# Kernel tuning notes

Measured on AMD Instinct MI355X. Metric: run time of the kernel, lower is better.

The kernel has to match this reference:

```python
import jax, jax.numpy as jnp
import numpy as np

_CLIP_MIN = 1e-6
_POS_ALPHA = 1e-3
RADIUS = 3
HALF_D = RADIUS * RADIUS  # 9: patch vector length per class
N_FINE, N_MID, N_HIGH = 19, 7, 3
LAMBDA = 0.5
LOSS_WEIGHT = 1.0
IGNORE = 255

_F2M = np.array([0,0,0,1,1,1,2,2,3,3,4,5,5,6,6,6,6,6,6], dtype=np.int64)
_M2H = np.array([0,0,1,1,1,2,2], dtype=np.int64)
_F2H = _M2H[_F2M]


def setup_inputs():
    key = jax.random.key(0)
    k1, k2, k3, k4 = jax.random.split(key, 4)
    B, H, W, D = 4, 512, 512, 256
    return {
        "step": 5000,
        "embedding": jax.random.normal(k1, (B, D, H // 8, W // 8), jnp.float32),
        "cls_score_before": jax.random.normal(k2, (B, N_FINE, H // 8, W // 8), jnp.float32),
        "cls_score": jax.random.normal(k3, (B, N_FINE + N_MID + N_HIGH, H, W), jnp.float32),
        "label": jax.random.randint(k4, (B, H, W), 0, N_FINE),
        "fine_to_mid": jnp.asarray(_F2M),
        "fine_to_high": jnp.asarray(_F2H),
    }


def _maxpool3(x):  # kernel=stride=3, VALID (rmi_pool_way=0)
    return jax.lax.reduce_window(x, -jnp.inf, jax.lax.max, (1, 1, 3, 3), (1, 1, 3, 3), "VALID")


def _map_get_pairs(la, pr, radius=RADIUS):
    b, c, h, w = la.shape
    nh, nw = h - radius + 1, w - radius + 1
    las = [la[:, :, y:y + nh, x:x + nw] for y in range(radius) for x in range(radius)]
    prs = [pr[:, :, y:y + nh, x:x + nw] for y in range(radius) for x in range(radius)]
    la_v = jnp.stack(las, axis=2).reshape(b, c, radius * radius, nh * nw)
    pr_v = jnp.stack(prs, axis=2).reshape(b, c, radius * radius, nh * nw)
    return la_v, pr_v


def _rmi_lower_bound(oh, probs, vmask):
    # oh, probs: [B,C,H,W]; vmask: [B,1,H,W]
    la = _maxpool3(oh * vmask)
    pr = _maxpool3(probs * vmask + _CLIP_MIN)
    la_v, pr_v = _map_get_pairs(la, pr)  # [B,C,half_d,N]
    la_v = jax.lax.stop_gradient(la_v)   # labels are detached in the original
    la_v = la_v - la_v.mean(axis=-1, keepdims=True)
    pr_v = pr_v - pr_v.mean(axis=-1, keepdims=True)
    diag = _POS_ALPHA * jnp.eye(HALF_D, dtype=la_v.dtype)
    pr_cov = jnp.einsum("bcdn,bcen->bcde", pr_v, pr_v) + diag
    la_cov = jnp.einsum("bcdn,bcen->bcde", la_v, la_v)
    la_pr = jnp.einsum("bcdn,bcen->bcde", la_v, pr_v)
    appro = la_cov - la_pr @ jnp.linalg.solve(pr_cov, jnp.swapaxes(la_pr, -1, -2)) + diag
    chol = jnp.linalg.cholesky(appro)
    logdet = 2.0 * jnp.sum(jnp.log(jnp.diagonal(chol, axis1=-2, axis2=-1) + 1e-8), axis=-1)  # [B,C]
    return jnp.sum(logdet.mean(axis=0) / HALF_D)


def _hiera_bce(oh, pos, neg, vmask):
    # positives judged against min-combined probs, negatives against max-combined probs
    loss = -(oh * jnp.log(pos + 1e-8) + (1.0 - oh) * jnp.log(1.0 - neg + 1e-8)) * vmask
    return loss.sum() / (vmask.sum() * oh.shape[1] + 1e-8)


def _forward(cls_score, label, fine_to_mid, fine_to_high):
    probs = jax.nn.sigmoid(cls_score.astype(jnp.float32))
    valid = (label != IGNORE)
    vmask = valid[:, None].astype(jnp.float32)  # [B,1,H,W]
    lf = jnp.where(valid, label, 0)
    lm = fine_to_mid[lf]
    lh = fine_to_high[lf]
    oh_f = jax.nn.one_hot(lf, N_FINE, axis=1, dtype=jnp.float32)
    oh_m = jax.nn.one_hot(lm, N_MID, axis=1, dtype=jnp.float32)
    oh_h = jax.nn.one_hot(lh, N_HIGH, axis=1, dtype=jnp.float32)
    MCMA = probs[:, :N_FINE]
    MCMB = probs[:, N_FINE:N_FINE + N_MID]
    MCMC = probs[:, N_FINE + N_MID:]
    # upward (max) hierarchy consistency
    segf = jax.ops.segment_max(jnp.moveaxis(MCMA, 1, 0), fine_to_mid, num_segments=N_MID)
    MCMB_c = jnp.maximum(jnp.moveaxis(segf, 0, 1), MCMB)
    mid_to_high = jnp.zeros((N_MID,), dtype=fine_to_high.dtype).at[fine_to_mid].set(fine_to_high)
    segm = jax.ops.segment_max(jnp.moveaxis(MCMB_c, 1, 0), mid_to_high, num_segments=N_HIGH)
    MCMC_c = jnp.maximum(jnp.moveaxis(segm, 0, 1), MCMC)
    # downward (min) hierarchy consistency
    MCLA = jnp.minimum(MCMA, MCMB[:, fine_to_mid])
    MCLB_c = jnp.minimum(MCMB, MCMC[:, mid_to_high])
    MCLC_c = MCMC
    total = 0.0
    for oh, pos, neg in ((oh_f, MCLA, MCMA), (oh_m, MCLB_c, MCMB_c), (oh_h, MCLC_c, MCMC_c)):
        bce = _hiera_bce(oh, pos, neg, vmask)
        rmi = _rmi_lower_bound(oh, pos, vmask)
        total = total + LAMBDA * bce + (1.0 - LAMBDA) * rmi
    return LOSS_WEIGHT * total


def reference(step, embedding, cls_score_before, cls_score, label, fine_to_mid, fine_to_high):
    # step / embedding / cls_score_before feed only the triplet branch (not in provided source)
    return _forward(cls_score, label, fine_to_mid, fine_to_high)
```

## Files before the change

### kernel.cpp

```cpp
#include <hip/hip_runtime.h>
#include <math.h>

namespace {
constexpr int NB = 4, NCHT = 29, NF = 19, NM = 7, NHI = 3;
constexpr int HH = 512, WW = 512;
constexpr int PH  = 170;
constexpr int NHW = 168;
constexpr int NS  = NHW * NHW;
constexpr int NBC = NB * NCHT;
constexpr int CROWS = 14;
constexpr int NCH2  = NHW / CROWS;

constexpr int F2M[NF] = {0,0,0,1,1,1,2,2,3,3,4,5,5,6,6,6,6,6,6};
constexpr int M2H[NM] = {0,0,1,1,1,2,2};
constexpr int F2H[NF] = {0,0,0,0,0,0,1,1,1,1,1,2,2,2,2,2,2,2,2};

constexpr unsigned long long packTbl(const int* a, int n) {
  unsigned long long p = 0;
  for (int i = 0; i < n; i++) p |= (unsigned long long)(a[i]) << (3 * i);
  return p;
}
constexpr unsigned long long PF2M = packTbl(F2M, NF);
constexpr unsigned long long PF2H = packTbl(F2H, NF);

constexpr int    WS_S1  = 16;
constexpr int    WS_COV = 4096;
constexpr int    WS_RED = 49152;
constexpr size_t WS_LA  = 65536;
constexpr size_t WS_PR  = WS_LA + (size_t)NBC * PH * PH;
constexpr size_t WS_ZERO_BYTES = (size_t)(WS_RED + 64 * 16) * 4;
}

#define GLOAD16(gsrc, ldst)                                                     \
  __builtin_amdgcn_global_load_lds(                                             \
      (const __attribute__((address_space(1))) void*)(gsrc),                    \
      (__attribute__((address_space(3))) void*)(ldst), 16, 0, 0)

__global__ __launch_bounds__(192)
void kA(const float* __restrict__ cls, const int* __restrict__ label,
        float* __restrict__ ws) {
  const int bx  = blockIdx.x;
  const int wy  = blockIdx.y;
  const int b   = blockIdx.z;
  const int tid = threadIdx.x;
  const int x0  = 48 * bx;
  const int y0  = 3 * wy;
  const int rmax = (wy == 170) ? 1 : 2;

  const int W4   = (bx < 10) ? 12 : 8;
  const int NCOL = 4 * W4;
  const int CST  = 3 * NCOL;
  const int NW   = (bx < 10) ? 16 : 10;

  __shared__ __align__(16) float    sPixF[NCHT * 144];
  __shared__ unsigned sMask[144];
  __shared__ float    sRed[4][3];

  {
    const int T3 = 3 * W4;
    const int total = NCHT * T3;
    for (int i = tid; i < total; i += 192) {
      const int c   = i / T3;
      const int rem = i - c * T3;
      const int r   = rem / W4;
      const int f   = rem - r * W4;
      const int rr  = (r <= rmax) ? r : rmax;
      const float* src =
          cls + ((size_t)(b * NCHT + c) * HH + (y0 + rr)) * WW + x0 + 4 * f;
      GLOAD16(src, &sPixF[4 * i]);
    }
  }
  __syncthreads();

  float bce0 = 0.f, bce1 = 0.f, bce2 = 0.f, cnt = 0.f;
  {
    const int p = tid;
    const int r = p / NCOL;
    if (p < CST && r <= rmax) {
      const int col = p - r * NCOL;
      const int lbl = label[((size_t)b * HH + (y0 + r)) * WW + x0 + col];
      const bool valid = (lbl != 255);
      const int lf = valid ? lbl : 0;
      const int lm = (int)((PF2M >> (3 * lf)) & 7ull);
      const int lh = (int)((PF2H >> (3 * lf)) & 7ull);
      const float vm = valid ? 1.f : 0.f;

      float pv[NCHT];
      #pragma unroll
      for (int c = 0; c < NCHT; c++)
        pv[c] = __builtin_amdgcn_rcpf(1.f + __expf(-sPixF[c * CST + p]));

      float segf[NM];
      #pragma unroll
      for (int m = 0; m < NM; m++) segf[m] = -1.f;
      #pragma unroll
      for (int f = 0; f < NF; f++) segf[F2M[f]] = fmaxf(segf[F2M[f]], pv[f]);
      float pBc[NM];
      #pragma unroll
      for (int m = 0; m < NM; m++) pBc[m] = fmaxf(segf[m], pv[NF + m]);
      float segm[NHI];
      #pragma unroll
      for (int k = 0; k < NHI; k++) segm[k] = -1.f;
      #pragma unroll
      for (int m = 0; m < NM; m++) segm[M2H[m]] = fmaxf(segm[M2H[m]], pBc[m]);
      float pCc[NHI];
      #pragma unroll
      for (int k = 0; k < NHI; k++) pCc[k] = fmaxf(segm[k], pv[NF + NM + k]);

      #pragma unroll
      for (int f = 0; f < NF; f++) {
        const float pos = fminf(pv[f], pv[NF + F2M[f]]);
        if (valid)
          bce0 -= __logf((f == lf) ? pos + 1e-8f : 1.f - pv[f] + 1e-8f);
        sPixF[f * CST + p] = pos * vm + 1e-6f;
      }
      #pragma unroll
      for (int m = 0; m < NM; m++) {
        const float pos = fminf(pv[NF + m], pv[NF + NM + M2H[m]]);
        if (valid)
          bce1 -= __logf((m == lm) ? pos + 1e-8f : 1.f - pBc[m] + 1e-8f);
        sPixF[(NF + m) * CST + p] = pos * vm + 1e-6f;
      }
      #pragma unroll
      for (int k = 0; k < NHI; k++) {
        const float pos = pv[NF + NM + k];
        if (valid)
          bce2 -= __logf((k == lh) ? pos + 1e-8f : 1.f - pCc[k] + 1e-8f);
        sPixF[(NF + NM + k) * CST + p] = pos * vm + 1e-6f;
      }
      sMask[p] = valid ? ((1u << lf) | (1u << (19 + lm)) | (1u << (26 + lh))) : 0u;
      cnt = vm;
    }
  }

  #pragma unroll
  for (int m = 32; m >= 1; m >>= 1) {
    bce0 += __shfl_xor(bce0, m);
    bce1 += __shfl_xor(bce1, m);
    bce2 += __shfl_xor(bce2, m);
    cnt  += __shfl_xor(cnt, m);
  }
  {
    const int wave = tid >> 6, lane = tid & 63;
    if (lane == 0) {
      sRed[0][wave] = bce0; sRed[1][wave] = bce1;
      sRed[2][wave] = bce2; sRed[3][wave] = cnt;
    }
  }
  __syncthreads();

  if (wy < 170) {
    float* la = ws + WS_LA;
    float* pr = ws + WS_PR;
    for (int t = tid; t < 16 * NCHT; t += 192) {
      const int c = t >> 4;
      const int w = t & 15;
      if (w < NW) {
        const int c0 = 3 * w;
        unsigned m = 0u;
        #pragma unroll
        for (int r = 0; r < 3; r++)
          m |= sMask[r * NCOL + c0] | sMask[r * NCOL + c0 + 1] |
               sMask[r * NCOL + c0 + 2];
        const size_t base =
            ((size_t)(b * NCHT) * PH + wy) * PH + (16 * bx + w);
        la[base + (size_t)c * PH * PH] = (float)((m >> c) & 1u);
        float v = 0.f;
        #pragma unroll
        for (int r = 0; r < 3; r++)
          v = fmaxf(v, fmaxf(fmaxf(sPixF[c * CST + r * NCOL + c0],
                                   sPixF[c * CST + r * NCOL + c0 + 1]),
                             sPixF[c * CST + r * NCOL + c0 + 2]));
        pr[base + (size_t)c * PH * PH] = v;
      }
    }
  }

  if (tid == 0) {
    const int slot = (bx + 11 * (wy + 171 * b)) & 63;
    float* dst = ws + WS_RED + slot * 16;
    atomicAdd(&dst[0], sRed[0][0] + sRed[0][1] + sRed[0][2]);
    atomicAdd(&dst[1], sRed[1][0] + sRed[1][1] + sRed[1][2]);
    atomicAdd(&dst[2], sRed[2][0] + sRed[2][1] + sRed[2][2]);
    atomicAdd(&dst[3], sRed[3][0] + sRed[3][1] + sRed[3][2]);
  }
}

__global__ __launch_bounds__(192)
void kCov(const float* __restrict__ ws_base, float* __restrict__ cov,
          float* __restrict__ s1out) {
  const int bc    = blockIdx.x / NCH2;
  const int chunk = blockIdx.x % NCH2;
  const int tid   = threadIdx.x;
  const int tile  = tid / 32;
  const int g     = tid % 32;
  const int ta = (tile < 3) ? 0 : ((tile < 5) ? 1 : 2);
  const int tb = (tile < 3) ? tile : ((tile < 5) ? tile - 2 : 2);
  const bool diag = (ta == tb);

  __shared__ __align__(16) float sA[16 * PH];
  __shared__ __align__(16) float sP[16 * PH];

  const int r0 = chunk * CROWS;
  const float* Ag = ws_base + WS_LA + (size_t)bc * PH * PH + (size_t)r0 * PH;
  const float* Pg = ws_base + WS_PR + (size_t)bc * PH * PH + (size_t)r0 * PH;
  for (int i = tid; i < (16 * PH) / 4; i += 192) {
    GLOAD16(Ag + 4 * i, &sA[4 * i]);
    GLOAD16(Pg + 4 * i, &sP[4 * i]);
  }
  __syncthreads();

  const float* baseA[6];
  const float* baseB[6];
  #pragma unroll
  for (int k = 0; k < 6; k++) {
    int r = 6 * ta + k, rr = r % 9;
    baseA[k] = ((r < 9) ? sA : sP) + (rr / 3) * PH + (rr % 3);
    int r2 = 6 * tb + k, rr2 = r2 % 9;
    baseB[k] = ((r2 < 9) ? sA : sP) + (rr2 / 3) * PH + (rr2 % 3);
  }

  float acc[6][6];
  #pragma unroll
  for (int k = 0; k < 6; k++)
    #pragma unroll
    for (int l = 0; l < 6; l++) acc[k][l] = 0.f;
  float sums[6];
  #pragma unroll
  for (int k = 0; k < 6; k++) sums[k] = 0.f;

  for (int lr = 0; lr < CROWS; lr++) {
    const int rowoff = lr * PH;
    for (int lc = g; lc < NHW; lc += 32) {
      float va[6], vb[6];
      #pragma unroll
      for (int k = 0; k < 6; k++) va[k] = baseA[k][rowoff + lc];
      #pragma unroll
      for (int k = 0; k < 6; k++) vb[k] = baseB[k][rowoff + lc];
      #pragma unroll
      for (int k = 0; k < 6; k++)
        #pragma unroll
        for (int l = 0; l < 6; l++) acc[k][l] = fmaf(va[k], vb[l], acc[k][l]);
      if (diag) {
        #pragma unroll
        for (int k = 0; k < 6; k++) sums[k] += va[k];
      }
    }
  }

  #pragma unroll
  for (int k = 0; k < 6; k++)
    #pragma unroll
    for (int l = 0; l < 6; l++) {
      float v = acc[k][l];
      #pragma unroll
      for (int m = 16; m >= 1; m >>= 1) v += __shfl_xor(v, m);
      acc[k][l] = v;
    }
  if (diag) {
    #pragma unroll
    for (int k = 0; k < 6; k++) {
      float v = sums[k];
      #pragma unroll
      for (int m = 16; m >= 1; m >>= 1) v += __shfl_xor(v, m);
      sums[k] = v;
    }
  }
  if (g == 0) {
    float* dst = cov + (size_t)bc * 324;
    #pragma unroll
    for (int k = 0; k < 6; k++)
      #pragma unroll
      for (int l = 0; l < 6; l++)
        atomicAdd(&dst[(6 * ta + k) * 18 + 6 * tb + l], acc[k][l]);
    if (diag) {
      #pragma unroll
      for (int k = 0; k < 6; k++)
        atomicAdd(&s1out[bc * 32 + 6 * ta + k], sums[k]);
    }
  }
}

__global__ __launch_bounds__(64)
void kSolve(const float* __restrict__ cov_all, const float* __restrict__ s1,
            float* __restrict__ acc) {
  const int bc   = blockIdx.x;
  const int lane = threadIdx.x;
  const float* cr = cov_all + (size_t)bc * 324;
  const double n = (double)NS;

  double mu[18];
  #pragma unroll
  for (int r = 0; r < 18; r++) mu[r] = (double)s1[bc * 32 + r] / n;
#define CC(i, j) ((double)cr[(i) * 18 + (j)] - n * mu[(i)] * mu[(j)])

  double row[9];
  #pragma unroll
  for (int j = 0; j < 9; j++)
    row[j] = (lane < 9 && j <= lane) ? CC(9 + j, 9 + lane) : 0.0;
  if (lane < 9) row[lane] += 1e-3;

  #pragma unroll
  for (int k = 0; k < 9; k++) {
    if (lane == k) {
      double s = row[k];
      #pragma unroll
      for (int m = 0; m < k; m++) s -= row[m] * row[m];
      row[k] = sqrt(fmax(s, 1e-300));
    }
    double rk[9];
    #pragma unroll
    for (int m = 0; m <= k; m++) rk[m] = __shfl(row[m], k);
    if (lane > k && lane < 9) {
      double s = row[k];
      #pragma unroll
      for (int m = 0; m < k; m++) s -= row[m] * rk[m];
      row[k] = s / rk[k];
    }
  }

  double Lm[9][9];
  #pragma unroll
  for (int i = 0; i < 9; i++)
    #pragma unroll
    for (int m = 0; m <= i; m++) Lm[i][m] = __shfl(row[m], i);

  double mc[9];
  #pragma unroll
  for (int r = 0; r < 9; r++) mc[r] = 0.0;
  if (lane < 9) {
    #pragma unroll
    for (int r = 0; r < 9; r++) {
      double s = CC(lane, 9 + r);
      #pragma unroll
      for (int m = 0; m < r; m++) s -= Lm[r][m] * mc[m];
      mc[r] = s / Lm[r][r];
    }
  }

  double a2[9];
  #pragma unroll
  for (int j = 0; j < 9; j++) a2[j] = 0.0;
  #pragma unroll
  for (int j = 0; j < 9; j++) {
    double mj[9];
    #pragma unroll
    for (int r = 0; r < 9; r++) mj[r] = __shfl(mc[r], j);
    double dot = 0.0;
    #pragma unroll
    for (int r = 0; r < 9; r++) dot += mc[r] * mj[r];
    if (lane < 9 && j <= lane)
      a2[j] = CC(j, lane) - dot + ((j == lane) ? 1e-3 : 0.0);
  }
#undef CC

  double myld = 0.0;
  #pragma unroll
  for (int k = 0; k < 9; k++) {
    if (lane == k) {
      double s = a2[k];
      #pragma unroll
      for (int m = 0; m < k; m++) s -= a2[m] * a2[m];
      double d = sqrt(fmax(s, 0.0));
      a2[k] = d;
      myld = 2.0 * log(d + 1e-8);
    }
    double rk[9];
    #pragma unroll
    for (int m = 0; m <= k; m++) rk[m] = __shfl(a2[m], k);
    if (lane > k && lane < 9) {
      double s = a2[k];
      #pragma unroll
      for (int m = 0; m < k; m++) s -= a2[m] * rk[m];
      a2[k] = s / rk[k];
    }
  }
  #pragma unroll
  for (int m = 32; m >= 1; m >>= 1) myld += __shfl_xor(myld, m);
  if (lane == 0) atomicAdd(&acc[4], (float)myld);
}

__global__ void kFin(const float* __restrict__ ws, float* __restrict__ out) {
  const int tid = threadIdx.x;
  const float* slot = ws + WS_RED + tid * 16;
  float b0 = slot[0], b1 = slot[1], b2 = slot[2], b3 = slot[3];
  #pragma unroll
  for (int m = 32; m >= 1; m >>= 1) {
    b0 += __shfl_xor(b0, m);
    b1 += __shfl_xor(b1, m);
    b2 += __shfl_xor(b2, m);
    b3 += __shfl_xor(b3, m);
  }
  if (tid == 0) {
    const double cnt = (double)b3;
    const double bce = 0.5 * ((double)b0 / (cnt * NF + 1e-8) +
                              (double)b1 / (cnt * NM + 1e-8) +
                              (double)b2 / (cnt * NHI + 1e-8));
    const double rmi = 0.5 * (double)ws[4] / (double)(NB * 9);
    out[0] = (float)(bce + rmi);
  }
}

extern "C" void kernel_launch(void* const* d_in, const int* in_sizes, int n_in,
                              void* d_out, int out_size, void* d_ws, size_t ws_size,
                              hipStream_t stream) {
  (void)in_sizes; (void)n_in; (void)out_size; (void)ws_size;
  const float* cls   = (const float*)d_in[3];
  const int*   label = (const int*)d_in[4];
  float* ws = (float*)d_ws;

  hipMemsetAsync(d_ws, 0, WS_ZERO_BYTES, stream);

  dim3 gA(11, 171, NB);
  kA<<<gA, 192, 0, stream>>>(cls, label, ws);
  kCov<<<NBC * NCH2, 192, 0, stream>>>(ws, ws + WS_COV, ws + WS_S1);
  kSolve<<<NBC, 64, 0, stream>>>(ws + WS_COV, ws + WS_S1, ws);
  kFin<<<1, 64, 0, stream>>>(ws, (float*)d_out);
}
```

Baseline: 126.8 us.

## Pool logits before sigmoid, use product-of-exp BCE, and tile pooled plane layout

The first kernel now max-pools raw logits and applies the sigmoid only to each pooled value, relying on sigmoid being monotonic. This cuts the per-pixel sigmoids to one per pooled cell. BCE is rewritten as log(1+exp(±x)) terms accumulated as products, so each group needs one log instead of one log per class. The pooled label and prediction planes move to a tiled layout (block × batch-channel × 16) so the writes are contiguous per block, and the covariance kernel gathers rows from that layout into padded LDS rows. Kernel A is also templated on tile width so the constants are known at compile time. Risks include float overflow of the accumulated products when logits are large, and scattered 16-byte gathers in the covariance load.

```diff
diff --git a/kernel.cpp b/kernel.cpp
--- a/kernel.cpp
+++ b/kernel.cpp
@@ -10,24 +10,26 @@
 constexpr int NBC = NB * NCHT;
 constexpr int CROWS = 14;
 constexpr int NCH2  = NHW / CROWS;
+constexpr int LDSW  = 176;
 
 constexpr int F2M[NF] = {0,0,0,1,1,1,2,2,3,3,4,5,5,6,6,6,6,6,6};
 constexpr int M2H[NM] = {0,0,1,1,1,2,2};
-constexpr int F2H[NF] = {0,0,0,0,0,0,1,1,1,1,1,2,2,2,2,2,2,2,2};
 
 constexpr unsigned long long packTbl(const int* a, int n) {
   unsigned long long p = 0;
   for (int i = 0; i < n; i++) p |= (unsigned long long)(a[i]) << (3 * i);
   return p;
 }
+constexpr int F2H_[NF] = {0,0,0,0,0,0,1,1,1,1,1,2,2,2,2,2,2,2,2};
 constexpr unsigned long long PF2M = packTbl(F2M, NF);
-constexpr unsigned long long PF2H = packTbl(F2H, NF);
+constexpr unsigned long long PF2H = packTbl(F2H_, NF);
 
 constexpr int    WS_S1  = 16;
 constexpr int    WS_COV = 4096;
 constexpr int    WS_RED = 49152;
+constexpr size_t PLANEF = (size_t)170 * 11 * NBC * 16;
 constexpr size_t WS_LA  = 65536;
-constexpr size_t WS_PR  = WS_LA + (size_t)NBC * PH * PH;
+constexpr size_t WS_PR  = WS_LA + PLANEF;
 constexpr size_t WS_ZERO_BYTES = (size_t)(WS_RED + 64 * 16) * 4;
 }
 
@@ -36,48 +38,35 @@
       (const __attribute__((address_space(1))) void*)(gsrc),                    \
       (__attribute__((address_space(3))) void*)(ldst), 16, 0, 0)
 
-__global__ __launch_bounds__(192)
-void kA(const float* __restrict__ cls, const int* __restrict__ label,
-        float* __restrict__ ws) {
-  const int bx  = blockIdx.x;
-  const int wy  = blockIdx.y;
-  const int b   = blockIdx.z;
-  const int tid = threadIdx.x;
-  const int x0  = 48 * bx;
-  const int y0  = 3 * wy;
+template <int W4>
+__device__ __forceinline__ void kA_body(
+    const int bx, const int wy, const int b, const int tid,
+    const float* __restrict__ cls, const int* __restrict__ label,
+    float* __restrict__ ws, float* sPixF, unsigned* sMask, float (*sRed)[3]) {
+  constexpr int NCOL = 4 * W4;
+  constexpr int CST  = 3 * NCOL;
+  constexpr int T3   = 3 * W4;
+  const int x0   = 48 * bx;
+  const int y0   = 3 * wy;
   const int rmax = (wy == 170) ? 1 : 2;
 
-  const int W4   = (bx < 10) ? 12 : 8;
-  const int NCOL = 4 * W4;
-  const int CST  = 3 * NCOL;
-  const int NW   = (bx < 10) ? 16 : 10;
-
-  __shared__ __align__(16) float    sPixF[NCHT * 144];
-  __shared__ unsigned sMask[144];
-  __shared__ float    sRed[4][3];
-
-  {
-    const int T3 = 3 * W4;
-    const int total = NCHT * T3;
-    for (int i = tid; i < total; i += 192) {
-      const int c   = i / T3;
-      const int rem = i - c * T3;
-      const int r   = rem / W4;
-      const int f   = rem - r * W4;
-      const int rr  = (r <= rmax) ? r : rmax;
-      const float* src =
-          cls + ((size_t)(b * NCHT + c) * HH + (y0 + rr)) * WW + x0 + 4 * f;
-      GLOAD16(src, &sPixF[4 * i]);
-    }
+  for (int i = tid; i < NCHT * T3; i += 192) {
+    const int c   = i / T3;
+    const int rem = i - c * T3;
+    const int r   = rem / W4;
+    const int f   = rem - r * W4;
+    const int rr  = (r <= rmax) ? r : rmax;
+    const float* src =
+        cls + ((size_t)(b * NCHT + c) * HH + (y0 + rr)) * WW + x0 + 4 * f;
+    GLOAD16(src, &sPixF[4 * i]);
   }
   __syncthreads();
 
   float bce0 = 0.f, bce1 = 0.f, bce2 = 0.f, cnt = 0.f;
-  {
-    const int p = tid;
-    const int r = p / NCOL;
-    if (p < CST && r <= rmax) {
-      const int col = p - r * NCOL;
+  if (tid < CST) {
+    const int r = tid / NCOL;
+    if (r <= rmax) {
+      const int col = tid - r * NCOL;
       const int lbl = label[((size_t)b * HH + (y0 + r)) * WW + x0 + col];
       const bool valid = (lbl != 255);
       const int lf = valid ? lbl : 0;
@@ -85,50 +74,54 @@
       const int lh = (int)((PF2H >> (3 * lf)) & 7ull);
       const float vm = valid ? 1.f : 0.f;
 
-      float pv[NCHT];
-      #pragma unroll
-      for (int c = 0; c < NCHT; c++)
-        pv[c] = __builtin_amdgcn_rcpf(1.f + __expf(-sPixF[c * CST + p]));
+      float x[NCHT];
+      #pragma unroll
+      for (int c = 0; c < NCHT; c++) x[c] = sPixF[c * CST + tid];
 
       float segf[NM];
       #pragma unroll
-      for (int m = 0; m < NM; m++) segf[m] = -1.f;
-      #pragma unroll
-      for (int f = 0; f < NF; f++) segf[F2M[f]] = fmaxf(segf[F2M[f]], pv[f]);
-      float pBc[NM];
-      #pragma unroll
-      for (int m = 0; m < NM; m++) pBc[m] = fmaxf(segf[m], pv[NF + m]);
+      for (int m = 0; m < NM; m++) segf[m] = -1e30f;
+      #pragma unroll
+      for (int f = 0; f < NF; f++) segf[F2M[f]] = fmaxf(segf[F2M[f]], x[f]);
+      float pBx[NM];
+      #pragma unroll
+      for (int m = 0; m < NM; m++) pBx[m] = fmaxf(segf[m], x[NF + m]);
       float segm[NHI];
       #pragma unroll
-      for (int k = 0; k < NHI; k++) segm[k] = -1.f;
-      #pragma unroll
-      for (int m = 0; m < NM; m++) segm[M2H[m]] = fmaxf(segm[M2H[m]], pBc[m]);
-      float pCc[NHI];
-      #pragma unroll
-      for (int k = 0; k < NHI; k++) pCc[k] = fmaxf(segm[k], pv[NF + NM + k]);
-
+      for (int k = 0; k < NHI; k++) segm[k] = -1e30f;
+      #pragma unroll
+      for (int m = 0; m < NM; m++) segm[M2H[m]] = fmaxf(segm[M2H[m]], pBx[m]);
+      float pCx[NHI];
+      #pragma unroll
+      for (int k = 0; k < NHI; k++) pCx[k] = fmaxf(segm[k], x[NF + NM + k]);
+
+      float prA = 1.f, prB = 1.f, prM = 1.f, prH = 1.f;
       #pragma unroll
       for (int f = 0; f < NF; f++) {
-        const float pos = fminf(pv[f], pv[NF + F2M[f]]);
-        if (valid)
-          bce0 -= __logf((f == lf) ? pos + 1e-8f : 1.f - pv[f] + 1e-8f);
-        sPixF[f * CST + p] = pos * vm + 1e-6f;
+        const float mx  = fminf(x[f], x[NF + F2M[f]]);
+        const float arg = (f == lf) ? -mx : x[f];
+        const float t = __builtin_fmaf(vm, __expf(arg), 1.f);
+        if (f < 10) prA *= t; else prB *= t;
+        sPixF[f * CST + tid] = valid ? mx : -1e30f;
       }
       #pragma unroll
       for (int m = 0; m < NM; m++) {
-        const float pos = fminf(pv[NF + m], pv[NF + NM + M2H[m]]);
-        if (valid)
-          bce1 -= __logf((m == lm) ? pos + 1e-8f : 1.f - pBc[m] + 1e-8f);
-        sPixF[(NF + m) * CST + p] = pos * vm + 1e-6f;
+        const float mx  = fminf(x[NF + m], x[NF + NM + M2H[m]]);
+        const float arg = (m == lm) ? -mx : pBx[m];
+        prM *= __builtin_fmaf(vm, __expf(arg), 1.f);
+        sPixF[(NF + m) * CST + tid] = valid ? mx : -1e30f;
       }
       #pragma unroll
       for (int k = 0; k < NHI; k++) {
-        const float pos = pv[NF + NM + k];
-        if (valid)
-          bce2 -= __logf((k == lh) ? pos + 1e-8f : 1.f - pCc[k] + 1e-8f);
-        sPixF[(NF + NM + k) * CST + p] = pos * vm + 1e-6f;
+        const float px  = x[NF + NM + k];
+        const float arg = (k == lh) ? -px : pCx[k];
+        prH *= __builtin_fmaf(vm, __expf(arg), 1.f);
+        sPixF[(NF + NM + k) * CST + tid] = valid ? px : -1e30f;
       }
-      sMask[p] = valid ? ((1u << lf) | (1u << (19 + lm)) | (1u << (26 + lh))) : 0u;
+      bce0 = __logf(prA) + __logf(prB);
+      bce1 = __logf(prM);
+      bce2 = __logf(prH);
+      sMask[tid] = valid ? ((1u << lf) | (1u << (19 + lm)) | (1u << (26 + lh))) : 0u;
       cnt = vm;
     }
   }
@@ -150,29 +143,25 @@
   __syncthreads();
 
   if (wy < 170) {
-    float* la = ws + WS_LA;
-    float* pr = ws + WS_PR;
-    for (int t = tid; t < 16 * NCHT; t += 192) {
-      const int c = t >> 4;
-      const int w = t & 15;
-      if (w < NW) {
-        const int c0 = 3 * w;
-        unsigned m = 0u;
-        #pragma unroll
-        for (int r = 0; r < 3; r++)
-          m |= sMask[r * NCOL + c0] | sMask[r * NCOL + c0 + 1] |
-               sMask[r * NCOL + c0 + 2];
-        const size_t base =
-            ((size_t)(b * NCHT) * PH + wy) * PH + (16 * bx + w);
-        la[base + (size_t)c * PH * PH] = (float)((m >> c) & 1u);
-        float v = 0.f;
-        #pragma unroll
-        for (int r = 0; r < 3; r++)
-          v = fmaxf(v, fmaxf(fmaxf(sPixF[c * CST + r * NCOL + c0],
-                                   sPixF[c * CST + r * NCOL + c0 + 1]),
-                             sPixF[c * CST + r * NCOL + c0 + 2]));
-        pr[base + (size_t)c * PH * PH] = v;
-      }
+    const size_t base = (size_t)(wy * 11 + bx) * 1856 + (size_t)b * 464;
+    float* la = ws + WS_LA + base;
+    float* pr = ws + WS_PR + base;
+    for (int t = tid; t < 464; t += 192) {
+      const int c = t >> 4, w = t & 15;
+      const int c0 = 3 * w;
+      unsigned m = 0u;
+      #pragma unroll
+      for (int r = 0; r < 3; r++)
+        m |= sMask[r * NCOL + c0] | sMask[r * NCOL + c0 + 1] |
+             sMask[r * NCOL + c0 + 2];
+      la[t] = (float)((m >> c) & 1u);
+      float v = -1e30f;
+      #pragma unroll
+      for (int r = 0; r < 3; r++)
+        v = fmaxf(v, fmaxf(fmaxf(sPixF[c * CST + r * NCOL + c0],
+                                 sPixF[c * CST + r * NCOL + c0 + 1]),
+                           sPixF[c * CST + r * NCOL + c0 + 2]));
+      pr[t] = __builtin_amdgcn_rcpf(1.f + __expf(-v)) + 1e-6f;
     }
   }
 
@@ -184,6 +173,19 @@
     atomicAdd(&dst[2], sRed[2][0] + sRed[2][1] + sRed[2][2]);
     atomicAdd(&dst[3], sRed[3][0] + sRed[3][1] + sRed[3][2]);
   }
+}
+
+__global__ __launch_bounds__(192)
+void kA(const float* __restrict__ cls, const int* __restrict__ label,
+        float* __restrict__ ws) {
+  __shared__ __align__(16) float sPixF[NCHT * 144];
+  __shared__ unsigned sMask[144];
+  __shared__ float    sRed[4][3];
+  const int bx = blockIdx.x, wy = blockIdx.y, b = blockIdx.z;
+  if (bx < 10)
+    kA_body<12>(bx, wy, b, threadIdx.x, cls, label, ws, sPixF, sMask, sRed);
+  else
+    kA_body<8>(bx, wy, b, threadIdx.x, cls, label, ws, sPixF, sMask, sRed);
 }
 
 __global__ __launch_bounds__(192)
@@ -198,15 +200,20 @@
   const int tb = (tile < 3) ? tile : ((tile < 5) ? tile - 2 : 2);
   const bool diag = (ta == tb);
 
-  __shared__ __align__(16) float sA[16 * PH];
-  __shared__ __align__(16) float sP[16 * PH];
+  __shared__ __align__(16) float sA[16 * LDSW];
+  __shared__ __align__(16) float sP[16 * LDSW];
 
   const int r0 = chunk * CROWS;
-  const float* Ag = ws_base + WS_LA + (size_t)bc * PH * PH + (size_t)r0 * PH;
-  const float* Pg = ws_base + WS_PR + (size_t)bc * PH * PH + (size_t)r0 * PH;
-  for (int i = tid; i < (16 * PH) / 4; i += 192) {
-    GLOAD16(Ag + 4 * i, &sA[4 * i]);
-    GLOAD16(Pg + 4 * i, &sP[4 * i]);
+  const float* laG = ws_base + WS_LA;
+  const float* prG = ws_base + WS_PR;
+  for (int i = tid; i < 16 * 44; i += 192) {
+    const int r  = i / 44;
+    const int ch = i - 44 * r;
+    const int wx = 4 * ch;
+    const size_t src =
+        (size_t)((r0 + r) * 11 + (wx >> 4)) * 1856 + (size_t)bc * 16 + (wx & 15);
+    GLOAD16(laG + src, &sA[4 * i]);
+    GLOAD16(prG + src, &sP[4 * i]);
   }
   __syncthreads();
 
@@ -215,9 +222,9 @@
   #pragma unroll
   for (int k = 0; k < 6; k++) {
     int r = 6 * ta + k, rr = r % 9;
-    baseA[k] = ((r < 9) ? sA : sP) + (rr / 3) * PH + (rr % 3);
+    baseA[k] = ((r < 9) ? sA : sP) + (rr / 3) * LDSW + (rr % 3);
     int r2 = 6 * tb + k, rr2 = r2 % 9;
-    baseB[k] = ((r2 < 9) ? sA : sP) + (rr2 / 3) * PH + (rr2 % 3);
+    baseB[k] = ((r2 < 9) ? sA : sP) + (rr2 / 3) * LDSW + (rr2 % 3);
   }
 
   float acc[6][6];
@@ -230,7 +237,7 @@
   for (int k = 0; k < 6; k++) sums[k] = 0.f;
 
   for (int lr = 0; lr < CROWS; lr++) {
-    const int rowoff = lr * PH;
+    const int rowoff = lr * LDSW;
     for (int lc = g; lc < NHW; lc += 32) {
       float va[6], vb[6];
       #pragma unroll
```

Measured after the change: 117.0 us. 1.08x faster.
